# Performance work log

Hardware: AMD Instinct MI355X
Metric: run time of the kernel (lower is better)

Reference implementation:

```python
import jax, jax.numpy as jnp
import numpy as np

# Architecture constants (from RUMamba.__init__ hard-coded Mamba2 config)
D_MODEL = 512
D_STATE = 128
D_CONV = 4
EXPAND = 4
HEADDIM = 32
D_INNER = EXPAND * D_MODEL            # 2048
NHEADS = D_INNER // HEADDIM           # 64
CONV_DIM = D_INNER + 2 * D_STATE      # 2304 (ngroups=1)
D_IN_PROJ = 2 * D_INNER + 2 * D_STATE + NHEADS  # 4416
NUM_CLASS = 2513
BATCH = 4
SEQ = 16


def setup_inputs() -> dict:
    key = jax.random.key(0)
    ks = jax.random.split(key, 8)
    inputs = jax.random.normal(ks[0], (BATCH, SEQ, D_MODEL), jnp.float32)
    in_proj_w = jax.random.normal(ks[1], (D_IN_PROJ, D_MODEL), jnp.float32) * 0.02
    conv_w = jax.random.normal(ks[2], (CONV_DIM, D_CONV), jnp.float32) * 0.2
    conv_b = jnp.zeros((CONV_DIM,), jnp.float32)
    # dt_bias initialized so softplus(dt_bias) ~ U(0.001, 0.1), as in Mamba2
    dt = jax.random.uniform(ks[3], (NHEADS,), jnp.float32, 0.001, 0.1)
    dt_bias = dt + jnp.log(-jnp.expm1(-dt))
    A_log = jnp.log(jax.random.uniform(ks[4], (NHEADS,), jnp.float32, 1.0, 16.0))
    cls_w = jax.random.normal(ks[5], (NUM_CLASS, HEADDIM * D_STATE), jnp.float32) * 0.02
    cls_b = jnp.zeros((NUM_CLASS,), jnp.float32)
    return {"inputs": inputs, "in_proj_w": in_proj_w, "conv_w": conv_w,
            "conv_b": conv_b, "dt_bias": dt_bias, "A_log": A_log,
            "cls_w": cls_w, "cls_b": cls_b}


def reference(inputs, in_proj_w, conv_w, conv_b, dt_bias, A_log, cls_w, cls_b):
    # inputs: (B, S, D) -> (S, B, D) as in forward's permute(1,0,2)
    seq = jnp.transpose(inputs, (1, 0, 2))
    S, B, _ = seq.shape

    # Shared in_proj for both rolling and unrolling (same Mamba math on inputs[t]).
    zxbcdt = jnp.einsum('sbd,ed->sbe', seq, in_proj_w)        # (S,B,4416)
    xBC_raw = zxbcdt[..., D_INNER:D_INNER + CONV_DIM]          # (S,B,2304)
    dt = jax.nn.softplus(zxbcdt[..., -NHEADS:] + dt_bias)      # (S,B,H)
    A = -jnp.exp(A_log)                                        # (H,)
    dA = jnp.exp(dt * A)                                       # (S,B,H)

    # --- Rolling pass: one length-1 Mamba call per timestep, SSM state carried,
    # conv state NOT carried -> causal conv on a length-1 seq uses only last tap.
    xBC_r = jax.nn.silu(xBC_raw * conv_w[:, -1] + conv_b)      # (S,B,2304)
    x_r = xBC_r[..., :D_INNER].reshape(S, B, NHEADS, HEADDIM)  # (S,B,H,P)
    B_r = xBC_r[..., D_INNER:D_INNER + D_STATE]                # (S,B,N)
    dBx = dt[..., None, None] * B_r[:, :, None, None, :] * x_r[..., None]  # (S,B,H,P,N)

    def roll_step(h, inp):
        dA_t, dBx_t = inp
        h = dA_t[..., None, None] * h + dBx_t
        return h, h

    h0 = jnp.zeros((B, NHEADS, HEADDIM, D_STATE), seq.dtype)
    _, states = jax.lax.scan(roll_step, h0, (dA, dBx))         # (S,B,H,P,N)

    # --- Unrolling pass: for each t, feed inputs[t] repeated (S - t + 1) times
    # starting from states[t]. Constant input => conv output only depends on
    # min(step, d_conv-1) via cumulative sums of reversed conv taps.
    cw = jnp.cumsum(conv_w[:, ::-1], axis=1)                   # (2304,4)
    t_idx = jnp.arange(S)

    def unroll_step(h, k):
        w_k = cw[:, jnp.minimum(k, D_CONV - 1)]                # (2304,)
        xBC_k = jax.nn.silu(xBC_raw * w_k + conv_b)            # (S,B,2304)
        x_k = xBC_k[..., :D_INNER].reshape(S, B, NHEADS, HEADDIM)
        B_k = xBC_k[..., D_INNER:D_INNER + D_STATE]
        h_new = dA[..., None, None] * h + \
            dt[..., None, None] * B_k[:, :, None, None, :] * x_k[..., None]
        active = (k <= S - t_idx)[:, None, None, None, None]   # length S - t + 1
        return jnp.where(active, h_new, h), None

    h_fin, _ = jax.lax.scan(unroll_step, states, jnp.arange(S + 1))  # (S,B,H,P,N)

    # Head-reduce to headdim*d_state = 4096 features, classify.
    feats = jnp.mean(h_fin, axis=2).reshape(S, B, HEADDIM * D_STATE)
    feats = jnp.transpose(feats, (1, 0, 2))                    # (B,S,4096)
    y = feats @ cls_w.T + cls_b                                # (B,S,num_class)
    return y
```

## Files before the change

kernel.cpp:

```cpp
#include <hip/hip_runtime.h>
#include <math.h>

#define S_LEN    16
#define NTOK     64
#define DMODEL   512
#define XB_COLS  2176
#define ZX_COLS  2240
#define NCLASS   2513
#define FEATDIM  4096
#define PD_STRIDE 2516

typedef float f4v __attribute__((ext_vector_type(4)));

__global__ __launch_bounds__(256) void k_fpart(const float* __restrict__ X,
                                               const float* __restrict__ W,
                                               float* __restrict__ partF) {
    const int tid = threadIdx.x;
    const int kf  = blockIdx.y;
    const int jb  = blockIdx.x * 64;
    const int k0  = kf * 64;

    __shared__ float A[64][64];
    __shared__ float B[64][64];

    {
        const int t  = tid >> 2;
        const int kq = tid & 3;
        const int xrow = (t & 3) * 16 + (t >> 2);
        const int e = (jb + t < XB_COLS) ? (2048 + jb + t) : (2176 + jb + t);
#pragma unroll
        for (int q = 0; q < 4; ++q) {
            const int kk = kq * 16 + q * 4;
            const float4 va = *reinterpret_cast<const float4*>(
                X + (size_t)xrow * DMODEL + k0 + kk);
            A[kk + 0][t] = va.x; A[kk + 1][t] = va.y;
            A[kk + 2][t] = va.z; A[kk + 3][t] = va.w;
            const float4 vb = *reinterpret_cast<const float4*>(
                W + (size_t)e * DMODEL + k0 + kk);
            B[kk + 0][t] = vb.x; B[kk + 1][t] = vb.y;
            B[kk + 2][t] = vb.z; B[kk + 3][t] = vb.w;
        }
    }
    __syncthreads();

    const int ti = tid >> 4;
    const int ci = tid & 15;
    float acc[4][4] = {{0.f}};
#pragma unroll 4
    for (int k = 0; k < 64; ++k) {
        const f4v a = *reinterpret_cast<const f4v*>(&A[k][ti * 4]);
        const f4v b = *reinterpret_cast<const f4v*>(&B[k][ci * 4]);
#pragma unroll
        for (int j = 0; j < 4; ++j)
#pragma unroll
            for (int l = 0; l < 4; ++l)
                acc[j][l] += a[j] * b[l];
    }
#pragma unroll
    for (int l = 0; l < 4; ++l) {
        f4v s; s[0] = acc[0][l]; s[1] = acc[1][l]; s[2] = acc[2][l]; s[3] = acc[3][l];
        *reinterpret_cast<f4v*>(
            partF + ((size_t)kf * ZX_COLS + jb + ci * 4 + l) * 64 + ti * 4) = s;
    }
}

__global__ __launch_bounds__(256) void k_fepi(const float* __restrict__ partF, int KF,
                                              const float* __restrict__ conv_w,
                                              const float* __restrict__ conv_b,
                                              const float* __restrict__ dt_bias,
                                              const float* __restrict__ A_log,
                                              float* __restrict__ u,
                                              float* __restrict__ aArr,
                                              float* __restrict__ dArr) {
    const int lane = threadIdx.x & 63;
    const int j    = blockIdx.x * 4 + (threadIdx.x >> 6);
    float acc = 0.f;
    for (int kf = 0; kf < KF; ++kf)
        acc += partF[((size_t)kf * ZX_COLS + j) * 64 + lane];

    if (j < XB_COLS) {
        const float4 cwv = *reinterpret_cast<const float4*>(conv_w + j * 4);
        const float cb = conv_b[j];
        float wk[4];
        wk[0] = cwv.w;
        wk[1] = wk[0] + cwv.z;
        wk[2] = wk[1] + cwv.y;
        wk[3] = wk[2] + cwv.x;
#pragma unroll
        for (int k = 0; k < 4; ++k) {
            const float v = acc * wk[k] + cb;
            u[((size_t)k * NTOK + lane) * XB_COLS + j] = v / (1.f + expf(-v));
        }
    } else {
        const int h = j - XB_COLS;
        const float x = acc + dt_bias[h];
        const float d = (x > 20.f) ? x : log1pf(expf(x));
        dArr[lane * 64 + h] = d;
        aArr[lane * 64 + h] = expf(-d * expf(A_log[h]));
    }
}

__global__ __launch_bounds__(256) void k_feats(const float* __restrict__ u,
                                               const float* __restrict__ aArr,
                                               const float* __restrict__ dArr,
                                               float* __restrict__ feats) {
    const int t = blockIdx.x >> 2;
    const int b = blockIdx.x & 3;
    const int tid = threadIdx.x;
    const int K = 16 - t;
    const int nvec = t + 5;

    __shared__ float q[16][64];
    __shared__ float cu[4][64];
    __shared__ float WV[20][32];
    __shared__ float Bv[20][128];

    if (tid < 64) {
        const int h = tid;
        const int mt = t * 4 + b;
        const float a   = aArr[mt * 64 + h];
        const float dtv = dArr[mt * 64 + h];
        float p = 1.f;
        float c3 = 0.f, c2 = 0.f, c1 = 0.f, c0 = 0.f, cs = 0.f;
        for (int j = 0; j <= K + 1; ++j) {
            if (j <= K - 3) c3 += p;
            if (j == K - 2) c2 = p;
            if (j == K - 1) c1 = p;
            if (j == K)     c0 = p;
            if (j == K + 1) cs = p;
            p *= a;
        }
        cu[0][h] = dtv * c0;
        cu[1][h] = dtv * c1;
        cu[2][h] = dtv * c2;
        cu[3][h] = dtv * c3;
        float prod = 1.f;
        for (int s = t; s >= 0; --s) {
            const int ms = s * 4 + b;
            q[s][h] = cs * prod * dArr[ms * 64 + h];
            prod *= aArr[ms * 64 + h];
        }
    }
    __syncthreads();

    {
        const int i = tid & 31;
        const int vs = tid >> 5;
        for (int v = vs; v < nvec; v += 8) {
            float acc = 0.f;
            if (v <= t) {
                const float* base = u + (size_t)(v * 4 + b) * XB_COLS;
                for (int h = 0; h < 64; ++h) acc += q[v][h] * base[h * 32 + i];
            } else {
                const int kk = v - t - 1;
                const float* base = u + ((size_t)kk * NTOK + t * 4 + b) * XB_COLS;
                for (int h = 0; h < 64; ++h) acc += cu[kk][h] * base[h * 32 + i];
            }
            WV[v][i] = acc;
        }
    }
    for (int x = tid; x < nvec * 128; x += 256) {
        const int v = x >> 7, n = x & 127;
        size_t src;
        if (v <= t) src = (size_t)(v * 4 + b) * XB_COLS + 2048 + n;
        else        src = ((size_t)(v - t - 1) * NTOK + t * 4 + b) * XB_COLS + 2048 + n;
        Bv[v][n] = u[src];
    }
    __syncthreads();

    {
        const int i  = tid >> 3;
        const int n0 = (tid & 7) * 16;
        const int r  = b * 16 + t;
        float acc[16];
#pragma unroll
        for (int nn = 0; nn < 16; ++nn) acc[nn] = 0.f;
        for (int v = 0; v < nvec; ++v) {
            const float wvv = WV[v][i];
#pragma unroll
            for (int nn = 0; nn < 16; ++nn) acc[nn] += wvv * Bv[v][n0 + nn];
        }
        float* dst = feats + (size_t)r * FEATDIM + i * 128 + n0;
#pragma unroll
        for (int qq = 0; qq < 4; ++qq) {
            float4 v4;
            v4.x = acc[qq * 4 + 0] * (1.f / 64.f);
            v4.y = acc[qq * 4 + 1] * (1.f / 64.f);
            v4.z = acc[qq * 4 + 2] * (1.f / 64.f);
            v4.w = acc[qq * 4 + 3] * (1.f / 64.f);
            *reinterpret_cast<float4*>(dst + qq * 4) = v4;
        }
    }
}

__global__ __launch_bounds__(64) void k_cls(const float* __restrict__ feats,
                                            const float* __restrict__ Wc,
                                            float* __restrict__ partialD) {
    const int tid   = threadIdx.x;
    const int ks    = blockIdx.y;
    const int cls0  = blockIdx.x * 64;
    const int chunk = FEATDIM / gridDim.y;
    const int nsub  = chunk / 64;

    __shared__ float A[64][64];
    __shared__ float B[64][64];

    const int ti = tid >> 3;
    const int ci = tid & 7;
    const int sq = tid & 15;
    const int sk = tid >> 4;

    float acc[8][8] = {{0.f}};

    for (int st = 0; st < nsub; ++st) {
        const int k0 = ks * chunk + st * 64;
        __syncthreads();
#pragma unroll
        for (int j = 0; j < 4; ++j) {
            const int kslot = sk + j * 4;
            float4 va[4];
#pragma unroll
            for (int r = 0; r < 4; ++r)
                va[r] = *reinterpret_cast<const float4*>(
                    feats + (size_t)(sq * 4 + r) * FEATDIM + k0 + kslot * 4);
#pragma unroll
            for (int s = 0; s < 4; ++s) {
                f4v w; w[0] = (&va[0].x)[s]; w[1] = (&va[1].x)[s];
                       w[2] = (&va[2].x)[s]; w[3] = (&va[3].x)[s];
                *reinterpret_cast<f4v*>(&A[kslot * 4 + s][sq * 4]) = w;
            }
            float4 vb[4];
#pragma unroll
            for (int r = 0; r < 4; ++r) {
                int cr = cls0 + sq * 4 + r; if (cr > NCLASS - 1) cr = NCLASS - 1;
                vb[r] = *reinterpret_cast<const float4*>(
                    Wc + (size_t)cr * FEATDIM + k0 + kslot * 4);
            }
#pragma unroll
            for (int s = 0; s < 4; ++s) {
                f4v w; w[0] = (&vb[0].x)[s]; w[1] = (&vb[1].x)[s];
                       w[2] = (&vb[2].x)[s]; w[3] = (&vb[3].x)[s];
                *reinterpret_cast<f4v*>(&B[kslot * 4 + s][sq * 4]) = w;
            }
        }
        __syncthreads();

#pragma unroll 8
        for (int k = 0; k < 64; ++k) {
            const f4v a0 = *reinterpret_cast<const f4v*>(&A[k][ti * 4]);
            const f4v a1 = *reinterpret_cast<const f4v*>(&A[k][32 + ti * 4]);
            const f4v b0 = *reinterpret_cast<const f4v*>(&B[k][ci * 4]);
            const f4v b1 = *reinterpret_cast<const f4v*>(&B[k][32 + ci * 4]);
#pragma unroll
            for (int j = 0; j < 4; ++j) {
#pragma unroll
                for (int l = 0; l < 4; ++l) {
                    acc[j][l]         += a0[j] * b0[l];
                    acc[j][l + 4]     += a0[j] * b1[l];
                    acc[j + 4][l]     += a1[j] * b0[l];
                    acc[j + 4][l + 4] += a1[j] * b1[l];
                }
            }
        }
    }

    const size_t obase = (size_t)ks * (NTOK * PD_STRIDE);
#pragma unroll
    for (int ta = 0; ta < 2; ++ta) {
#pragma unroll
        for (int j = 0; j < 4; ++j) {
            const int row = ta * 32 + ti * 4 + j;
#pragma unroll
            for (int cb = 0; cb < 2; ++cb) {
                const int c = cls0 + cb * 32 + ci * 4;
                f4v s;
#pragma unroll
                for (int l = 0; l < 4; ++l) s[l] = acc[ta * 4 + j][cb * 4 + l];
                float* dst = partialD + obase + (size_t)row * PD_STRIDE + c;
                if (c + 3 < NCLASS) {
                    *reinterpret_cast<f4v*>(dst) = s;
                } else {
#pragma unroll
                    for (int l = 0; l < 4; ++l)
                        if (c + l < NCLASS) dst[l] = s[l];
                }
            }
        }
    }
}

__global__ void k_out(const float* __restrict__ partialD, const float* __restrict__ cls_b,
                      float* __restrict__ out, int KC) {
    const int bx = blockIdx.x;
    const int r  = bx / 10;
    const int c  = (bx % 10) * 256 + threadIdx.x;
    if (c >= NCLASS) return;
    float s = cls_b[c];
    for (int ks = 0; ks < KC; ++ks)
        s += partialD[(size_t)ks * (NTOK * PD_STRIDE) + (size_t)r * PD_STRIDE + c];
    out[(size_t)r * NCLASS + c] = s;
}

extern "C" void kernel_launch(void* const* d_in, const int* in_sizes, int n_in,
                              void* d_out, int out_size, void* d_ws, size_t ws_size,
                              hipStream_t stream) {
    const float* inputs  = (const float*)d_in[0];
    const float* in_proj = (const float*)d_in[1];
    const float* conv_w  = (const float*)d_in[2];
    const float* conv_b  = (const float*)d_in[3];
    const float* dt_bias = (const float*)d_in[4];
    const float* A_log   = (const float*)d_in[5];
    const float* cls_w   = (const float*)d_in[6];
    const float* cls_b   = (const float*)d_in[7];
    float* out = (float*)d_out;

    float* ws = (float*)d_ws;
    float* aArr    = ws;
    float* dArr    = ws + 4096;
    float* feats   = ws + 8192;
    float* scr     = ws + 270336;
    float* u       = scr;
    float* partF   = scr + 557056;
    float* partialD = scr;

    int KC;
    if (ws_size >= 11386880u) KC = 16;
    else                      KC = 8;

    k_fpart <<<dim3(35, 8), 256, 0, stream>>>(inputs, in_proj, partF);
    k_fepi  <<<560, 256, 0, stream>>>(partF, 8, conv_w, conv_b, dt_bias, A_log,
                                      u, aArr, dArr);
    k_feats <<<64, 256, 0, stream>>>(u, aArr, dArr, feats);
    k_cls   <<<dim3(40, KC), 64, 0, stream>>>(feats, cls_w, partialD);
    k_out   <<<640, 256, 0, stream>>>(partialD, cls_b, out, KC);
}
```

Baseline: 69.91 us.

## Split classifier K-tile across four waves per block with per-wave partial outputs

The classifier GEMM block grows from one wave to four. Each wave computes a quarter of every 64-wide K tile and writes its own partial-sum slab, and the final reduction kernel sums four times as many partials. The tile load is rewritten so each thread loads one row segment with scalar transposed LDS stores. The K-split count is now chosen from workspace size with new thresholds, so the total partial count may change. The goal is more waves per CU to hide the load latency of the bandwidth-bound classifier weight stream, at the cost of more partial-sum traffic in the reduction and possible LDS bank conflicts in the transposed stores.

After: 73.79 us. 1.06x slower.

```diff
diff --git a/kernel.cpp b/kernel.cpp
--- a/kernel.cpp
+++ b/kernel.cpp
@@ -193,10 +193,12 @@
     }
 }
 
-__global__ __launch_bounds__(64) void k_cls(const float* __restrict__ feats,
-                                            const float* __restrict__ Wc,
-                                            float* __restrict__ partialD) {
+__global__ __launch_bounds__(256) void k_cls(const float* __restrict__ feats,
+                                             const float* __restrict__ Wc,
+                                             float* __restrict__ partialD) {
     const int tid   = threadIdx.x;
+    const int lane  = tid & 63;
+    const int wv    = tid >> 6;
     const int ks    = blockIdx.y;
     const int cls0  = blockIdx.x * 64;
     const int chunk = FEATDIM / gridDim.y;
@@ -205,52 +207,40 @@
     __shared__ float A[64][64];
     __shared__ float B[64][64];
 
-    const int ti = tid >> 3;
-    const int ci = tid & 7;
-    const int sq = tid & 15;
-    const int sk = tid >> 4;
+    const int ti = lane >> 3;
+    const int ci = lane & 7;
 
     float acc[8][8] = {{0.f}};
 
     for (int st = 0; st < nsub; ++st) {
         const int k0 = ks * chunk + st * 64;
         __syncthreads();
-#pragma unroll
-        for (int j = 0; j < 4; ++j) {
-            const int kslot = sk + j * 4;
-            float4 va[4];
-#pragma unroll
-            for (int r = 0; r < 4; ++r)
-                va[r] = *reinterpret_cast<const float4*>(
-                    feats + (size_t)(sq * 4 + r) * FEATDIM + k0 + kslot * 4);
-#pragma unroll
-            for (int s = 0; s < 4; ++s) {
-                f4v w; w[0] = (&va[0].x)[s]; w[1] = (&va[1].x)[s];
-                       w[2] = (&va[2].x)[s]; w[3] = (&va[3].x)[s];
-                *reinterpret_cast<f4v*>(&A[kslot * 4 + s][sq * 4]) = w;
+        {
+            const int t  = tid >> 2;
+            const int kq = tid & 3;
+            int cr = cls0 + t; if (cr > NCLASS - 1) cr = NCLASS - 1;
+#pragma unroll
+            for (int q = 0; q < 4; ++q) {
+                const int kk = kq * 16 + q * 4;
+                const float4 va = *reinterpret_cast<const float4*>(
+                    feats + (size_t)t * FEATDIM + k0 + kk);
+                A[kk + 0][t] = va.x; A[kk + 1][t] = va.y;
+                A[kk + 2][t] = va.z; A[kk + 3][t] = va.w;
+                const float4 vb = *reinterpret_cast<const float4*>(
+                    Wc + (size_t)cr * FEATDIM + k0 + kk);
+                B[kk + 0][t] = vb.x; B[kk + 1][t] = vb.y;
+                B[kk + 2][t] = vb.z; B[kk + 3][t] = vb.w;
             }
-            float4 vb[4];
-#pragma unroll
-            for (int r = 0; r < 4; ++r) {
-                int cr = cls0 + sq * 4 + r; if (cr > NCLASS - 1) cr = NCLASS - 1;
-                vb[r] = *reinterpret_cast<const float4*>(
-                    Wc + (size_t)cr * FEATDIM + k0 + kslot * 4);
-            }
-#pragma unroll
-            for (int s = 0; s < 4; ++s) {
-                f4v w; w[0] = (&vb[0].x)[s]; w[1] = (&vb[1].x)[s];
-                       w[2] = (&vb[2].x)[s]; w[3] = (&vb[3].x)[s];
-                *reinterpret_cast<f4v*>(&B[kslot * 4 + s][sq * 4]) = w;
-            }
         }
         __syncthreads();
 
-#pragma unroll 8
-        for (int k = 0; k < 64; ++k) {
-            const f4v a0 = *reinterpret_cast<const f4v*>(&A[k][ti * 4]);
-            const f4v a1 = *reinterpret_cast<const f4v*>(&A[k][32 + ti * 4]);
-            const f4v b0 = *reinterpret_cast<const f4v*>(&B[k][ci * 4]);
-            const f4v b1 = *reinterpret_cast<const f4v*>(&B[k][32 + ci * 4]);
+#pragma unroll 4
+        for (int k = 0; k < 16; ++k) {
+            const int kk = wv * 16 + k;
+            const f4v a0 = *reinterpret_cast<const f4v*>(&A[kk][ti * 4]);
+            const f4v a1 = *reinterpret_cast<const f4v*>(&A[kk][32 + ti * 4]);
+            const f4v b0 = *reinterpret_cast<const f4v*>(&B[kk][ci * 4]);
+            const f4v b1 = *reinterpret_cast<const f4v*>(&B[kk][32 + ci * 4]);
 #pragma unroll
             for (int j = 0; j < 4; ++j) {
 #pragma unroll
@@ -264,7 +254,7 @@
         }
     }
 
-    const size_t obase = (size_t)ks * (NTOK * PD_STRIDE);
+    const size_t obase = (size_t)(ks * 4 + wv) * (NTOK * PD_STRIDE);
 #pragma unroll
     for (int ta = 0; ta < 2; ++ta) {
 #pragma unroll
@@ -290,14 +280,14 @@
 }
 
 __global__ void k_out(const float* __restrict__ partialD, const float* __restrict__ cls_b,
-                      float* __restrict__ out, int KC) {
+                      float* __restrict__ out, int NP) {
     const int bx = blockIdx.x;
     const int r  = bx / 10;
     const int c  = (bx % 10) * 256 + threadIdx.x;
     if (c >= NCLASS) return;
     float s = cls_b[c];
-    for (int ks = 0; ks < KC; ++ks)
-        s += partialD[(size_t)ks * (NTOK * PD_STRIDE) + (size_t)r * PD_STRIDE + c];
+    for (int p = 0; p < NP; ++p)
+        s += partialD[(size_t)p * (NTOK * PD_STRIDE) + (size_t)r * PD_STRIDE + c];
     out[(size_t)r * NCLASS + c] = s;
 }
 
@@ -324,13 +314,15 @@
     float* partialD = scr;
 
     int KC;
-    if (ws_size >= 11386880u) KC = 16;
-    else                      KC = 8;
+    if      (ws_size >= 42303488u) KC = 16;
+    else if (ws_size >= 21692416u) KC = 8;
+    else if (ws_size >= 11386880u) KC = 4;
+    else                           KC = 2;
 
     k_fpart <<<dim3(35, 8), 256, 0, stream>>>(inputs, in_proj, partF);
     k_fepi  <<<560, 256, 0, stream>>>(partF, 8, conv_w, conv_b, dt_bias, A_log,
                                       u, aArr, dArr);
     k_feats <<<64, 256, 0, stream>>>(u, aArr, dArr, feats);
-    k_cls   <<<dim3(40, KC), 64, 0, stream>>>(feats, cls_w, partialD);
-    k_out   <<<640, 256, 0, stream>>>(partialD, cls_b, out, KC);
-}
+    k_cls   <<<dim3(40, KC), 256, 0, stream>>>(feats, cls_w, partialD);
+    k_out   <<<640, 256, 0, stream>>>(partialD, cls_b, out, 4 * KC);
+}
```
